# Performance work log

Measured on AMD Instinct MI355X. Metric: run time of the kernel, lower is better.

The kernel has to match this reference:

```python
import jax, jax.numpy as jnp
from jax import lax
import numpy as np

EPS = 1e-8

def squash(x, axis=-1):
    sq = jnp.sum(x * x, axis=axis, keepdims=True)
    return sq / (1.0 + sq) * x / (jnp.sqrt(sq) + EPS)

def conv1d(x, w, b):
    # x: [B, Cin, L], w: [Cout, Cin, K]
    y = lax.conv_general_dilated(x, w, (1,), 'VALID',
                                 dimension_numbers=('NCH', 'OIH', 'NCH'))
    return y + b[None, :, None]

def setup_inputs() -> dict:
    key = jax.random.key(0)
    ks = jax.random.split(key, 6)
    B = 4096
    x = jax.random.normal(ks[0], (B, 50, 128), dtype=jnp.float32)
    conv1_w = jax.random.normal(ks[1], (50, 128, 9), dtype=jnp.float32) * (1.0 / np.sqrt(128 * 9))
    conv1_b = jnp.zeros((50,), dtype=jnp.float32)
    pconv_w = jax.random.normal(ks[2], (64, 42, 3), dtype=jnp.float32) * (1.0 / np.sqrt(42 * 3))
    pconv_b = jnp.zeros((64,), dtype=jnp.float32)
    W = 0.01 * jax.random.normal(ks[3], (5, 384, 16, 8), dtype=jnp.float32)
    return {"x": x, "conv1_w": conv1_w, "conv1_b": conv1_b,
            "pconv_w": pconv_w, "pconv_b": pconv_b, "W": W}

def reference(x, conv1_w, conv1_b, pconv_w, pconv_b, W):
    B = x.shape[0]
    NUM_ROUTING = 3
    # conv + relu: [B,50,128] -> [B,128,50] -> conv -> [B,50,42] -> permute -> [B,42,50]
    h = conv1d(jnp.transpose(x, (0, 2, 1)), conv1_w, conv1_b)
    h = jnp.transpose(jax.nn.relu(h), (0, 2, 1))  # [B,42,50]
    # primary caps: conv1d -> [B,64,48] -> reshape [B,384,8] -> squash
    p = conv1d(h, pconv_w, pconv_b)
    u = squash(p.reshape(B, -1, 8), axis=-1)  # [B,384,8]
    # u_hat[b,o,c,d] = W[o,c,d,i] * u[b,c,i]
    u_hat = jnp.einsum('ocdi,bci->bocd', W, u)  # [B,5,384,16]
    tu = lax.stop_gradient(u_hat)
    b = jnp.zeros((B, 5, 384, 1), dtype=u_hat.dtype)
    for _ in range(NUM_ROUTING - 1):
        c = jax.nn.softmax(b, axis=1)            # [B,5,384,1]
        s = jnp.sum(c * tu, axis=2)              # [B,5,16]
        v = squash(s)                            # [B,5,16]
        uv = jnp.einsum('bocd,bod->boc', tu, v)[..., None]
        b = b + uv
    c = jax.nn.softmax(b, axis=1)
    s = jnp.sum(c * u_hat, axis=2)
    v = squash(s)  # [B,5,16]
    return v
```

## Files before the change

### kernel.cpp

```cpp
#include <hip/hip_runtime.h>
#include <hip/hip_bf16.h>

typedef unsigned short ushort_t;
typedef _Float16 h2 __attribute__((ext_vector_type(2)));
typedef _Float16 half4_t __attribute__((ext_vector_type(4)));
typedef _Float16 half8_t __attribute__((ext_vector_type(8)));
typedef float f32x4 __attribute__((ext_vector_type(4)));
#define EPSQ 1e-8f

__device__ __forceinline__ float fdot2f(h2 a, h2 b, float c) {
#if __has_builtin(__builtin_amdgcn_fdot2)
  return __builtin_amdgcn_fdot2(a, b, c, false);
#else
  return fmaf((float)a.x, (float)b.x, fmaf((float)a.y, (float)b.y, c));
#endif
}
__device__ __forceinline__ h2 bc_h2(unsigned int v) { return __builtin_bit_cast(h2, v); }
__device__ __forceinline__ unsigned int bc_u32(h2 v) { return __builtin_bit_cast(unsigned int, v); }
__device__ __forceinline__ ushort_t bc_u16(_Float16 v) { return __builtin_bit_cast(ushort_t, v); }


__global__ __launch_bounds__(256) void k0_prep(
    const float* __restrict__ w1, const float* __restrict__ pw,
    const float* __restrict__ Wf,
    _Float16* __restrict__ wc16, _Float16* __restrict__ pwB16,
    _Float16* __restrict__ Whs)
{
  int i = blockIdx.x * 256 + threadIdx.x;
  if (i < 73728) {
    int c  = i / 8192;
    int r  = i % 8192;
    int co = r >> 7;
    int k  = r & 127;
    wc16[i] = (co < 50) ? (_Float16)w1[co*1152 + k*9 + c] : (_Float16)0.f;
  }
  if (i < 10240) {
    int co2 = i / 160, kk = i % 160;
    int k = kk / 48, ci = kk % 48;
    float v = (k < 3 && ci < 42) ? pw[co2*126 + ci*3 + k] : 0.f;
    pwB16[i] = (_Float16)v;
  }
  {
    int i8 = i & 7;
    int r  = i >> 3;
    int d  = r & 15;
    int rc = r >> 4;
    int c  = rc % 384;
    int o  = rc / 384;
    Whs[(((o*16 + d)*384) + c)*8 + i8] = (_Float16)Wf[i];
  }
}

__global__ __launch_bounds__(256) void k12_mfma(
    const float* __restrict__ x, const float* __restrict__ b1,
    const float* __restrict__ b2, const _Float16* __restrict__ wc16,
    const _Float16* __restrict__ pwB16, ushort_t* __restrict__ u16)
{
  __shared__ float smem[19728];
  _Float16* xh   = (_Float16*)smem;
  _Float16* hr16 = (_Float16*)smem;
  _Float16* pB   = (_Float16*)smem + 8736;
  float*    pbuf = smem + 9744;

  const int tid   = threadIdx.x;
  const int w     = tid >> 6;
  const int lane  = tid & 63;
  const int lc    = lane & 15;
  const int qd    = lane >> 4;
  const int gbase = blockIdx.x * 3;

  for (int j = tid; j < 4800; j += 256) {
    int g = j / 1600, r = j - g*1600;
    int p = r >> 5, q = r & 31;
    int bb = gbase + g; if (bb > 4095) bb = 4095;
    float4 v = *(const float4*)(x + bb*6400 + p*128 + q*4);
    half4_t hv = {(_Float16)v.x, (_Float16)v.y, (_Float16)v.z, (_Float16)v.w};
    *(half4_t*)(xh + g*6800 + p*136 + q*4) = hv;
  }
  {
    const uint4* wg = (const uint4*)wc16;
    uint4* dst = (uint4*)(xh + 20400);
#pragma unroll
    for (int it = 0; it < 4; ++it) {
      int f = it*256 + tid;
      dst[(f >> 4)*17 + (f & 15)] = wg[f];
    }
  }

  const _Float16* abase[2];
#pragma unroll
  for (int tm = 0; tm < 2; ++tm) {
    int m = 32*w + 16*tm + lc;
    if (m > 125) m = 125;
    int g = m / 42, l = m - g*42;
    abase[tm] = xh + g*6800 + l*136 + qd*8;
  }

  f32x4 acc[2][4];
#pragma unroll
  for (int tm = 0; tm < 2; ++tm)
#pragma unroll
    for (int tn = 0; tn < 4; ++tn)
      acc[tm][tn] = (f32x4){0.f, 0.f, 0.f, 0.f};

  __syncthreads();

  uint4 pf[4];
  for (int c = 0; c < 9; ++c) {
    if (c < 8) {
      const uint4* wg = (const uint4*)wc16 + (c + 1)*1024;
#pragma unroll
      for (int it = 0; it < 4; ++it) pf[it] = wg[it*256 + tid];
    }
    const _Float16* Bb = xh + 20400 + (c & 1)*8704;
    const _Float16* a0 = abase[0] + c*136;
    const _Float16* a1 = abase[1] + c*136;
#pragma unroll
    for (int kk = 0; kk < 128; kk += 32) {
      half8_t av0 = *(const half8_t*)(a0 + kk);
      half8_t av1 = *(const half8_t*)(a1 + kk);
#pragma unroll
      for (int tn = 0; tn < 4; ++tn) {
        half8_t bv = *(const half8_t*)(Bb + (16*tn + lc)*136 + qd*8 + kk);
        acc[0][tn] = __builtin_amdgcn_mfma_f32_16x16x32_f16(av0, bv, acc[0][tn], 0, 0, 0);
        acc[1][tn] = __builtin_amdgcn_mfma_f32_16x16x32_f16(av1, bv, acc[1][tn], 0, 0, 0);
      }
    }
    __syncthreads();
    if (c < 8) {
      uint4* dst = (uint4*)(xh + 20400 + ((c + 1) & 1)*8704);
#pragma unroll
      for (int it = 0; it < 4; ++it) {
        int f = it*256 + tid;
        dst[(f >> 4)*17 + (f & 15)] = pf[it];
      }
      __syncthreads();
    }
  }

  for (int j = tid; j < 4368; j += 256) smem[j] = 0.f;
  {
    const uint4* pg = (const uint4*)pwB16;
    uint4* dst = (uint4*)pB;
    for (int f = tid; f < 1280; f += 256) {
      int row = f / 20, cc = f - row*20;
      dst[row*21 + cc] = pg[f];
    }
  }
  __syncthreads();

#pragma unroll
  for (int tm = 0; tm < 2; ++tm) {
    int mb = 32*w + 16*tm + 4*qd;
#pragma unroll
    for (int tn = 0; tn < 4; ++tn) {
      int co = 16*tn + lc;
      if (co < 50) {
        float bias = b1[co];
#pragma unroll
        for (int r = 0; r < 4; ++r) {
          int m = mb + r;
          if (m < 126) {
            int g = m / 42, l = m - g*42;
            hr16[g*2912 + co*56 + l] = (_Float16)fmaxf(acc[tm][tn][r] + bias, 0.f);
          }
        }
      }
    }
  }
  __syncthreads();

  f32x4 acc2[3][4];
#pragma unroll
  for (int tm = 0; tm < 3; ++tm)
#pragma unroll
    for (int tn = 0; tn < 4; ++tn)
      acc2[tm][tn] = (f32x4){0.f, 0.f, 0.f, 0.f};

#pragma unroll
  for (int kc = 0; kc < 5; ++kc) {
    int kk0 = kc*32 + qd*8;
    int k   = (kk0 >= 144) ? 3 : (kk0 >= 96) ? 2 : (kk0 >= 48) ? 1 : 0;
    int ci0 = kk0 - k*48;
    half8_t bv[4];
#pragma unroll
    for (int tn = 0; tn < 4; ++tn)
      bv[tn] = *(const half8_t*)(pB + (16*tn + lc)*168 + kk0);
#pragma unroll
    for (int tm = 0; tm < 3; ++tm) {
      int T = w + 4*tm; int Tc = (T < 9) ? T : 8;
      int g = Tc/3, l2 = (Tc - g*3)*16 + lc;
      half8_t av = *(const half8_t*)(hr16 + g*2912 + (l2 + k)*56 + ci0);
#pragma unroll
      for (int tn = 0; tn < 4; ++tn)
        acc2[tm][tn] = __builtin_amdgcn_mfma_f32_16x16x32_f16(av, bv[tn], acc2[tm][tn], 0, 0, 0);
    }
  }

#pragma unroll
  for (int tm = 0; tm < 3; ++tm) {
    int T = w + 4*tm;
    if (T < 9) {
      int g = T/3, l2b = (T - g*3)*16;
#pragma unroll
      for (int tn = 0; tn < 4; ++tn) {
        int co2 = 16*tn + lc;
        float bias2 = b2[co2];
#pragma unroll
        for (int r = 0; r < 4; ++r) {
          int l2 = l2b + 4*qd + r;
          pbuf[g*3328 + co2*52 + l2] = acc2[tm][tn][r] + bias2;
        }
      }
    }
  }
  __syncthreads();

  for (int idx = tid; idx < 1152; idx += 256) {
    int g = idx / 384, cap = idx - g*384;
    int bb = gbase + g;
    if (bb < 4096) {
      int co2 = cap / 6, gg = cap - co2*6;
      const float* pp = pbuf + g*3328 + co2*52 + gg*8;
      float4 a0 = *(const float4*)pp;
      float4 a1 = *(const float4*)(pp + 4);
      float sq = a0.x*a0.x + a0.y*a0.y + a0.z*a0.z + a0.w*a0.w
               + a1.x*a1.x + a1.y*a1.y + a1.z*a1.z + a1.w*a1.w;
      float sc = sq / ((1.f + sq) * (sqrtf(sq) + EPSQ));
      h2 p0 = {(_Float16)(a0.x*sc), (_Float16)(a0.y*sc)};
      h2 p1 = {(_Float16)(a0.z*sc), (_Float16)(a0.w*sc)};
      h2 p2 = {(_Float16)(a1.x*sc), (_Float16)(a1.y*sc)};
      h2 p3 = {(_Float16)(a1.z*sc), (_Float16)(a1.w*sc)};
      *(uint4*)(u16 + ((size_t)bb*384 + cap)*8) =
          make_uint4(bc_u32(p0), bc_u32(p1), bc_u32(p2), bc_u32(p3));
    }
  }
}

__global__ __launch_bounds__(384) void k3_route(
    const ushort_t* __restrict__ u16, const _Float16* __restrict__ Whs,
    float* __restrict__ out)
{
  __shared__ __align__(16) float part[6][80];
  __shared__ __align__(16) ushort_t svh16[80];

  const int t    = threadIdx.x;
  const int b    = blockIdx.x;
  const int w    = t >> 6;
  const int lane = t & 63;
  const int jmap = ((lane & 1) << 3) | ((lane & 2) << 1) | ((lane & 4) >> 1) | ((lane & 8) >> 3);

  uint4 uu0 = *(const uint4*)(u16 + ((size_t)b*384 + t)*8);
  h2 ua0[4] = {bc_h2(uu0.x), bc_h2(uu0.y), bc_h2(uu0.z), bc_h2(uu0.w)};

  h2 uhreg[40];
  const uint4* wb = (const uint4*)Whs;
#pragma unroll
  for (int o = 0; o < 5; ++o) {
    const uint4* wp = wb + (size_t)(o*16)*384 + t;
#pragma unroll
    for (int dd = 0; dd < 8; ++dd) {
      uint4 w0 = wp[(size_t)(2*dd)*384];
      uint4 w1 = wp[(size_t)(2*dd + 1)*384];
      float s00 = fdot2f(bc_h2(w0.x), ua0[0], fdot2f(bc_h2(w0.y), ua0[1],
                  fdot2f(bc_h2(w0.z), ua0[2], fdot2f(bc_h2(w0.w), ua0[3], 0.f))));
      float s10 = fdot2f(bc_h2(w1.x), ua0[0], fdot2f(bc_h2(w1.y), ua0[1],
                  fdot2f(bc_h2(w1.z), ua0[2], fdot2f(bc_h2(w1.w), ua0[3], 0.f))));
      uhreg[o*8 + dd] = (h2){(_Float16)s00, (_Float16)s10};
    }
  }

  float lg[5] = {0.f, 0.f, 0.f, 0.f, 0.f};

  const bool s0 = (lane & 1) != 0;
  const bool s1 = (lane & 2) != 0;
  const bool s2 = (lane & 4) != 0;
  const bool s3 = (lane & 8) != 0;

  for (int it = 0; it < 3; ++it) {
    float co[5];
    {
      float m = fmaxf(fmaxf(fmaxf(lg[0],lg[1]),fmaxf(lg[2],lg[3])),lg[4]);
      float Z = 0.f;
#pragma unroll
      for (int o = 0; o < 5; ++o) { co[o] = __expf(lg[o]-m); Z += co[o]; }
      float inv = 1.f / Z;
#pragma unroll
      for (int o = 0; o < 5; ++o) co[o] *= inv;
    }

#pragma unroll
    for (int o = 0; o < 5; ++o) {
      float v16[16];
#pragma unroll
      for (int dd = 0; dd < 8; ++dd) {
        h2 uh = uhreg[o*8 + dd];
        v16[2*dd]     = co[o] * (float)uh.x;
        v16[2*dd + 1] = co[o] * (float)uh.y;
      }
      float v8[8];
#pragma unroll
      for (int i = 0; i < 8; ++i) {
        float keep = s0 ? v16[i+8] : v16[i];
        float send = s0 ? v16[i]   : v16[i+8];
        v8[i] = keep + __shfl_xor(send, 1);
      }
      float v4[4];
#pragma unroll
      for (int i = 0; i < 4; ++i) {
        float keep = s1 ? v8[i+4] : v8[i];
        float send = s1 ? v8[i]   : v8[i+4];
        v4[i] = keep + __shfl_xor(send, 2);
      }
      float v2[2];
#pragma unroll
      for (int i = 0; i < 2; ++i) {
        float keep = s2 ? v2[0]*0.f + v4[i+2] : v4[i];
        float send = s2 ? v4[i]   : v4[i+2];
        v2[i] = (s2 ? v4[i+2] : v4[i]) + __shfl_xor(send, 4);
      }
      float v1;
      {
        float keep = s3 ? v2[1] : v2[0];
        float send = s3 ? v2[0] : v2[1];
        v1 = keep + __shfl_xor(send, 8);
      }
      v1 += __shfl_xor(v1, 16);
      v1 += __shfl_xor(v1, 32);
      if (lane < 16) part[w][o*16 + jmap] = v1;
    }
    __syncthreads();

    if (t < 80) {
      float s = part[0][t] + part[1][t] + part[2][t]
              + part[3][t] + part[4][t] + part[5][t];
      float sq = s * s;
      sq += __shfl_xor(sq, 1);
      sq += __shfl_xor(sq, 2);
      sq += __shfl_xor(sq, 4);
      sq += __shfl_xor(sq, 8);
      float f = sq / ((1.f + sq) * (sqrtf(sq) + EPSQ));
      if (it == 2) out[(size_t)b*80 + t] = s * f;
      else         svh16[t] = bc_u16((_Float16)(s * f));
    }
    __syncthreads();

    if (it < 2) {
#pragma unroll
      for (int o = 0; o < 5; ++o) {
        uint4 sa = *(const uint4*)&svh16[o*16];
        uint4 sb = *(const uint4*)&svh16[o*16 + 8];
        float dv = 0.f;
        dv = fdot2f(uhreg[o*8+0], bc_h2(sa.x), dv);
        dv = fdot2f(uhreg[o*8+1], bc_h2(sa.y), dv);
        dv = fdot2f(uhreg[o*8+2], bc_h2(sa.z), dv);
        dv = fdot2f(uhreg[o*8+3], bc_h2(sa.w), dv);
        dv = fdot2f(uhreg[o*8+4], bc_h2(sb.x), dv);
        dv = fdot2f(uhreg[o*8+5], bc_h2(sb.y), dv);
        dv = fdot2f(uhreg[o*8+6], bc_h2(sb.z), dv);
        dv = fdot2f(uhreg[o*8+7], bc_h2(sb.w), dv);
        lg[o] += dv;
      }
    }
  }
}

extern "C" void kernel_launch(void* const* d_in, const int* in_sizes, int n_in,
                              void* d_out, int out_size, void* d_ws, size_t ws_size,
                              hipStream_t stream) {
  const float* x  = (const float*)d_in[0];
  const float* w1 = (const float*)d_in[1];
  const float* b1 = (const float*)d_in[2];
  const float* pw = (const float*)d_in[3];
  const float* b2 = (const float*)d_in[4];
  const float* Wf = (const float*)d_in[5];
  float* out = (float*)d_out;
  char* ws = (char*)d_ws;

  _Float16* wc16  = (_Float16*)(ws);
  _Float16* pwB16 = (_Float16*)(ws + 147456);
  _Float16* Whs   = (_Float16*)(ws + 167936);
  ushort_t* u16   = (ushort_t*)(ws + 659456);

  k0_prep<<<960, 256, 0, stream>>>(w1, pw, Wf, wc16, pwB16, Whs);
  k12_mfma<<<1366, 256, 0, stream>>>(x, b1, b2, wc16, pwB16, u16);
  k3_route<<<4096, 384, 0, stream>>>(u16, Whs, out);
}
```

Before: 455.1 us.

## Process three batch samples per routing block to reuse W loads

```diff
diff --git a/kernel.cpp b/kernel.cpp
--- a/kernel.cpp
+++ b/kernel.cpp
@@ -241,19 +241,25 @@
     const ushort_t* __restrict__ u16, const _Float16* __restrict__ Whs,
     float* __restrict__ out)
 {
-  __shared__ __align__(16) float part[6][80];
-  __shared__ __align__(16) ushort_t svh16[80];
+  __shared__ __align__(16) float part[3][6][80];
+  __shared__ __align__(16) ushort_t svh16[3][80];
 
   const int t    = threadIdx.x;
-  const int b    = blockIdx.x;
+  const int b0   = blockIdx.x * 3;
   const int w    = t >> 6;
   const int lane = t & 63;
   const int jmap = ((lane & 1) << 3) | ((lane & 2) << 1) | ((lane & 4) >> 1) | ((lane & 8) >> 3);
 
-  uint4 uu0 = *(const uint4*)(u16 + ((size_t)b*384 + t)*8);
-  h2 ua0[4] = {bc_h2(uu0.x), bc_h2(uu0.y), bc_h2(uu0.z), bc_h2(uu0.w)};
-
-  h2 uhreg[40];
+  h2 ua[3][4];
+#pragma unroll
+  for (int bb = 0; bb < 3; ++bb) {
+    int bidx = b0 + bb; if (bidx > 4095) bidx = 4095;
+    uint4 uu = *(const uint4*)(u16 + ((size_t)bidx*384 + t)*8);
+    ua[bb][0] = bc_h2(uu.x); ua[bb][1] = bc_h2(uu.y);
+    ua[bb][2] = bc_h2(uu.z); ua[bb][3] = bc_h2(uu.w);
+  }
+
+  h2 uhreg[3][40];
   const uint4* wb = (const uint4*)Whs;
 #pragma unroll
   for (int o = 0; o < 5; ++o) {
@@ -262,15 +268,18 @@
     for (int dd = 0; dd < 8; ++dd) {
       uint4 w0 = wp[(size_t)(2*dd)*384];
       uint4 w1 = wp[(size_t)(2*dd + 1)*384];
-      float s00 = fdot2f(bc_h2(w0.x), ua0[0], fdot2f(bc_h2(w0.y), ua0[1],
-                  fdot2f(bc_h2(w0.z), ua0[2], fdot2f(bc_h2(w0.w), ua0[3], 0.f))));
-      float s10 = fdot2f(bc_h2(w1.x), ua0[0], fdot2f(bc_h2(w1.y), ua0[1],
-                  fdot2f(bc_h2(w1.z), ua0[2], fdot2f(bc_h2(w1.w), ua0[3], 0.f))));
-      uhreg[o*8 + dd] = (h2){(_Float16)s00, (_Float16)s10};
-    }
-  }
-
-  float lg[5] = {0.f, 0.f, 0.f, 0.f, 0.f};
+#pragma unroll
+      for (int bb = 0; bb < 3; ++bb) {
+        float s00 = fdot2f(bc_h2(w0.x), ua[bb][0], fdot2f(bc_h2(w0.y), ua[bb][1],
+                    fdot2f(bc_h2(w0.z), ua[bb][2], fdot2f(bc_h2(w0.w), ua[bb][3], 0.f))));
+        float s10 = fdot2f(bc_h2(w1.x), ua[bb][0], fdot2f(bc_h2(w1.y), ua[bb][1],
+                    fdot2f(bc_h2(w1.z), ua[bb][2], fdot2f(bc_h2(w1.w), ua[bb][3], 0.f))));
+        uhreg[bb][o*8 + dd] = (h2){(_Float16)s00, (_Float16)s10};
+      }
+    }
+  }
+
+  float lg[3][5] = {{0,0,0,0,0},{0,0,0,0,0},{0,0,0,0,0}};
 
   const bool s0 = (lane & 1) != 0;
   const bool s1 = (lane & 2) != 0;
@@ -278,88 +287,98 @@
   const bool s3 = (lane & 8) != 0;
 
   for (int it = 0; it < 3; ++it) {
-    float co[5];
-    {
-      float m = fmaxf(fmaxf(fmaxf(lg[0],lg[1]),fmaxf(lg[2],lg[3])),lg[4]);
-      float Z = 0.f;
-#pragma unroll
-      for (int o = 0; o < 5; ++o) { co[o] = __expf(lg[o]-m); Z += co[o]; }
-      float inv = 1.f / Z;
-#pragma unroll
-      for (int o = 0; o < 5; ++o) co[o] *= inv;
-    }
-
-#pragma unroll
-    for (int o = 0; o < 5; ++o) {
-      float v16[16];
-#pragma unroll
-      for (int dd = 0; dd < 8; ++dd) {
-        h2 uh = uhreg[o*8 + dd];
-        v16[2*dd]     = co[o] * (float)uh.x;
-        v16[2*dd + 1] = co[o] * (float)uh.y;
-      }
-      float v8[8];
-#pragma unroll
-      for (int i = 0; i < 8; ++i) {
-        float keep = s0 ? v16[i+8] : v16[i];
-        float send = s0 ? v16[i]   : v16[i+8];
-        v8[i] = keep + __shfl_xor(send, 1);
-      }
-      float v4[4];
-#pragma unroll
-      for (int i = 0; i < 4; ++i) {
-        float keep = s1 ? v8[i+4] : v8[i];
-        float send = s1 ? v8[i]   : v8[i+4];
-        v4[i] = keep + __shfl_xor(send, 2);
-      }
-      float v2[2];
-#pragma unroll
-      for (int i = 0; i < 2; ++i) {
-        float keep = s2 ? v2[0]*0.f + v4[i+2] : v4[i];
-        float send = s2 ? v4[i]   : v4[i+2];
-        v2[i] = (s2 ? v4[i+2] : v4[i]) + __shfl_xor(send, 4);
-      }
-      float v1;
+#pragma unroll
+    for (int bb = 0; bb < 3; ++bb) {
+      float co[5];
       {
-        float keep = s3 ? v2[1] : v2[0];
-        float send = s3 ? v2[0] : v2[1];
-        v1 = keep + __shfl_xor(send, 8);
-      }
-      v1 += __shfl_xor(v1, 16);
-      v1 += __shfl_xor(v1, 32);
-      if (lane < 16) part[w][o*16 + jmap] = v1;
+        float m = fmaxf(fmaxf(fmaxf(lg[bb][0],lg[bb][1]),fmaxf(lg[bb][2],lg[bb][3])),lg[bb][4]);
+        float Z = 0.f;
+#pragma unroll
+        for (int o = 0; o < 5; ++o) { co[o] = __expf(lg[bb][o]-m); Z += co[o]; }
+        float inv = 1.f / Z;
+#pragma unroll
+        for (int o = 0; o < 5; ++o) co[o] *= inv;
+      }
+
+#pragma unroll
+      for (int o = 0; o < 5; ++o) {
+        float v16[16];
+#pragma unroll
+        for (int dd = 0; dd < 8; ++dd) {
+          h2 uh = uhreg[bb][o*8 + dd];
+          v16[2*dd]     = co[o] * (float)uh.x;
+          v16[2*dd + 1] = co[o] * (float)uh.y;
+        }
+        float v8[8];
+#pragma unroll
+        for (int i = 0; i < 8; ++i) {
+          float keep = s0 ? v16[i+8] : v16[i];
+          float send = s0 ? v16[i]   : v16[i+8];
+          v8[i] = keep + __shfl_xor(send, 1);
+        }
+        float v4[4];
+#pragma unroll
+        for (int i = 0; i < 4; ++i) {
+          float keep = s1 ? v8[i+4] : v8[i];
+          float send = s1 ? v8[i]   : v8[i+4];
+          v4[i] = keep + __shfl_xor(send, 2);
+        }
+        float v2[2];
+#pragma unroll
+        for (int i = 0; i < 2; ++i) {
+          float keep = s2 ? v4[i+2] : v4[i];
+          float send = s2 ? v4[i]   : v4[i+2];
+          v2[i] = keep + __shfl_xor(send, 4);
+        }
+        float v1;
+        {
+          float keep = s3 ? v2[1] : v2[0];
+          float send = s3 ? v2[0] : v2[1];
+          v1 = keep + __shfl_xor(send, 8);
+        }
+        v1 += __shfl_xor(v1, 16);
+        v1 += __shfl_xor(v1, 32);
+        if (lane < 16) part[bb][w][o*16 + jmap] = v1;
+      }
     }
     __syncthreads();
 
-    if (t < 80) {
-      float s = part[0][t] + part[1][t] + part[2][t]
-              + part[3][t] + part[4][t] + part[5][t];
+    if (t < 240) {
+      int bb = t / 80, idx = t - bb*80;
+      float s = part[bb][0][idx] + part[bb][1][idx] + part[bb][2][idx]
+              + part[bb][3][idx] + part[bb][4][idx] + part[bb][5][idx];
       float sq = s * s;
       sq += __shfl_xor(sq, 1);
       sq += __shfl_xor(sq, 2);
       sq += __shfl_xor(sq, 4);
       sq += __shfl_xor(sq, 8);
       float f = sq / ((1.f + sq) * (sqrtf(sq) + EPSQ));
-      if (it == 2) out[(size_t)b*80 + t] = s * f;
-      else         svh16[t] = bc_u16((_Float16)(s * f));
+      if (it == 2) {
+        if (b0 + bb < 4096) out[(size_t)(b0 + bb)*80 + idx] = s * f;
+      } else {
+        svh16[bb][idx] = bc_u16((_Float16)(s * f));
+      }
     }
     __syncthreads();
 
     if (it < 2) {
 #pragma unroll
-      for (int o = 0; o < 5; ++o) {
-        uint4 sa = *(const uint4*)&svh16[o*16];
-        uint4 sb = *(const uint4*)&svh16[o*16 + 8];
-        float dv = 0.f;
-        dv = fdot2f(uhreg[o*8+0], bc_h2(sa.x), dv);
-        dv = fdot2f(uhreg[o*8+1], bc_h2(sa.y), dv);
-        dv = fdot2f(uhreg[o*8+2], bc_h2(sa.z), dv);
-        dv = fdot2f(uhreg[o*8+3], bc_h2(sa.w), dv);
-        dv = fdot2f(uhreg[o*8+4], bc_h2(sb.x), dv);
-        dv = fdot2f(uhreg[o*8+5], bc_h2(sb.y), dv);
-        dv = fdot2f(uhreg[o*8+6], bc_h2(sb.z), dv);
-        dv = fdot2f(uhreg[o*8+7], bc_h2(sb.w), dv);
-        lg[o] += dv;
+      for (int bb = 0; bb < 3; ++bb) {
+#pragma unroll
+        for (int o = 0; o < 5; ++o) {
+          uint4 sa = *(const uint4*)&svh16[bb][o*16];
+          uint4 sb = *(const uint4*)&svh16[bb][o*16 + 8];
+          float dv = 0.f;
+          dv = fdot2f(uhreg[bb][o*8+0], bc_h2(sa.x), dv);
+          dv = fdot2f(uhreg[bb][o*8+1], bc_h2(sa.y), dv);
+          dv = fdot2f(uhreg[bb][o*8+2], bc_h2(sa.z), dv);
+          dv = fdot2f(uhreg[bb][o*8+3], bc_h2(sa.w), dv);
+          dv = fdot2f(uhreg[bb][o*8+4], bc_h2(sb.x), dv);
+          dv = fdot2f(uhreg[bb][o*8+5], bc_h2(sb.y), dv);
+          dv = fdot2f(uhreg[bb][o*8+6], bc_h2(sb.z), dv);
+          dv = fdot2f(uhreg[bb][o*8+7], bc_h2(sb.w), dv);
+          lg[bb][o] += dv;
+        }
       }
     }
   }
@@ -384,5 +403,5 @@
 
   k0_prep<<<960, 256, 0, stream>>>(w1, pw, Wf, wc16, pwB16, Whs);
   k12_mfma<<<1366, 256, 0, stream>>>(x, b1, b2, wc16, pwB16, u16);
-  k3_route<<<4096, 384, 0, stream>>>(u16, Whs, out);
+  k3_route<<<1366, 384, 0, stream>>>(u16, Whs, out);
 }
```

Result: slower. 915.9 us (+101.2%).
